# Performance work log

Measured on AMD Instinct MI355X. Metric: run time of the kernel, lower is better.

Reference implementation:

```python
import jax, jax.numpy as jnp
import numpy as np

BATCH, NEURONS, N_FEAT, IN_DIM, OUT_DIM = 256, 1024, 1024, 256, 128


def setup_inputs() -> dict:
    key = jax.random.key(0)
    kx, kg, kv, kw = jax.random.split(key, 4)
    x = jax.random.normal(kx, (BATCH, N_FEAT, IN_DIM), dtype=jnp.float32)
    G = jax.random.normal(kg, (NEURONS, N_FEAT), dtype=jnp.float32)
    # Original initializes v, w to zeros; use randn so outputs/grads are non-trivial.
    v = jax.random.normal(kv, (NEURONS, IN_DIM, OUT_DIM), dtype=jnp.float32)
    w = jax.random.normal(kw, (NEURONS, IN_DIM, OUT_DIM), dtype=jnp.float32)
    return {"x": x, "G": G, "v": v, "w": w}


def reference(x, G, v, w):
    # Original math: out[i,m] = sum_{j,k,l} G[j,k] * x[i,k,l] * (v - w)[j,l,m]
    # Reordered contraction: first G @ x (sum over feature axis k),
    # avoiding the quadratic (batch, neurons, n, in_dim) intermediate.
    Gx = jnp.einsum('jk,ikl->ijl', G, x)          # (batch, neurons, in_dim)
    return jnp.einsum('ijl,jlm->im', Gx, v - w)    # (batch, out_dim)
```

## Files before the change

kernel.cpp:

```cpp
#include <hip/hip_runtime.h>
#include <hip/hip_bf16.h>


typedef __attribute__((ext_vector_type(8))) short bf16x8;
typedef __attribute__((ext_vector_type(4))) float f32x4;

#define AS1C(p) ((const __attribute__((address_space(1))) void*)(p))
#define AS3(p)  ((__attribute__((address_space(3))) void*)(p))

__device__ __forceinline__ unsigned short f2bf(float f) {
    unsigned u = __float_as_uint(f);
    unsigned r = u + 0x7fffu + ((u >> 16) & 1u);
    return (unsigned short)(r >> 16);
}

__global__ void prep_G(const float* __restrict__ G, unsigned short* __restrict__ Gt) {
    __shared__ float tile[32][33];
    int k0 = blockIdx.x * 32, j0 = blockIdx.y * 32;
    int tx = threadIdx.x, ty = threadIdx.y;
    #pragma unroll
    for (int r = 0; r < 32; r += 8)
        tile[ty + r][tx] = G[(size_t)(j0 + ty + r) * 1024 + k0 + tx];
    __syncthreads();
    #pragma unroll
    for (int r = 0; r < 32; r += 8)
        Gt[(size_t)(k0 + ty + r) * 1024 + j0 + tx] = f2bf(tile[tx][ty + r]);
}

__global__ void prep_D(const float* __restrict__ v, const float* __restrict__ w,
                       unsigned short* __restrict__ Dt) {
    __shared__ unsigned short tile[64][132];
    int j0 = blockIdx.x * 64;
    int l  = blockIdx.y;
    int t  = threadIdx.x;
    #pragma unroll
    for (int it = 0; it < 8; ++it) {
        int f = it * 256 + t;
        int j = f >> 5;
        int c4 = (f & 31) * 4;
        size_t g = (size_t)(j0 + j) * 32768 + (size_t)l * 128 + c4;
        float4 a = *(const float4*)(v + g);
        float4 b = *(const float4*)(w + g);
        unsigned short h[4] = { f2bf(a.x - b.x), f2bf(a.y - b.y),
                                f2bf(a.z - b.z), f2bf(a.w - b.w) };
        *(uint2*)(&tile[j][c4]) = *(uint2*)h;
    }
    __syncthreads();
    int m = t >> 1, half = t & 1;
    unsigned short vals[32];
    #pragma unroll
    for (int q = 0; q < 32; ++q) vals[q] = tile[half * 32 + q][m];
    size_t dst = ((size_t)m * 256 + l) * 1024 + j0 + half * 32;
    #pragma unroll
    for (int p = 0; p < 4; ++p)
        *(uint4*)(Dt + dst + p * 8) = *(uint4*)(vals + p * 8);
}

__global__ __launch_bounds__(256) void gemm1(const unsigned short* __restrict__ Gt,
                                             const unsigned short* __restrict__ Dt,
                                             unsigned short* __restrict__ Tt) {
    __shared__ __align__(16) unsigned short As[128 * 32];
    __shared__ __align__(16) unsigned short Bs[128 * 32];
    __shared__ __align__(16) unsigned short Ct[64][136];
    int tid = threadIdx.x, wv = tid >> 6, lane = tid & 63;
    int k0 = blockIdx.x * 128, n0 = blockIdx.y * 128;
    int ldrow = lane >> 2, ldcol = (lane & 3) * 8;
    int wr = (wv >> 1) * 64, wc = (wv & 1) * 64;
    int quad = lane >> 4, l15 = lane & 15;

    f32x4 acc[4][4] = {};

    for (int j0 = 0; j0 < 1024; j0 += 32) {
        #pragma unroll
        for (int i = 0; i < 2; ++i) {
            int r = wv * 32 + i * 16;
            __builtin_amdgcn_global_load_lds(
                AS1C(Gt + (size_t)(k0 + r + ldrow) * 1024 + j0 + ldcol),
                AS3(As + r * 32), 16, 0, 0);
            __builtin_amdgcn_global_load_lds(
                AS1C(Dt + (size_t)(n0 + r + ldrow) * 1024 + j0 + ldcol),
                AS3(Bs + r * 32), 16, 0, 0);
        }
        __syncthreads();
        bf16x8 a[4], b[4];
        #pragma unroll
        for (int rt = 0; rt < 4; ++rt)
            a[rt] = *(const bf16x8*)(As + (wr + rt * 16 + l15) * 32 + quad * 8);
        #pragma unroll
        for (int ct = 0; ct < 4; ++ct)
            b[ct] = *(const bf16x8*)(Bs + (wc + ct * 16 + l15) * 32 + quad * 8);
        #pragma unroll
        for (int rt = 0; rt < 4; ++rt)
            #pragma unroll
            for (int ct = 0; ct < 4; ++ct)
                acc[rt][ct] = __builtin_amdgcn_mfma_f32_16x16x32_bf16(a[rt], b[ct], acc[rt][ct], 0, 0, 0);
        __syncthreads();
    }
    int mQ = n0 >> 8, l0 = n0 & 255;
    #pragma unroll
    for (int h = 0; h < 2; ++h) {
        if ((wv >> 1) == h) {
            #pragma unroll
            for (int rt = 0; rt < 4; ++rt)
                #pragma unroll
                for (int ct = 0; ct < 4; ++ct)
                    #pragma unroll
                    for (int r = 0; r < 4; ++r)
                        Ct[rt * 16 + quad * 4 + r][wc + ct * 16 + l15] = f2bf(acc[rt][ct][r]);
        }
        __syncthreads();
        int row = tid >> 2, qo = (tid & 3) * 32;
        size_t dst = (size_t)mQ * 262144 + (size_t)(k0 + h * 64 + row) * 256 + l0 + qo;
        uint4 d0 = *(uint4*)(&Ct[row][qo]);
        uint4 d1 = *(uint4*)(&Ct[row][qo + 8]);
        uint4 d2 = *(uint4*)(&Ct[row][qo + 16]);
        uint4 d3 = *(uint4*)(&Ct[row][qo + 24]);
        *(uint4*)(Tt + dst)      = d0;
        *(uint4*)(Tt + dst + 8)  = d1;
        *(uint4*)(Tt + dst + 16) = d2;
        *(uint4*)(Tt + dst + 24) = d3;
        __syncthreads();
    }
}

__global__ __launch_bounds__(256, 4) void gemm2(const float* __restrict__ x,
                                                const unsigned short* __restrict__ Tt,
                                                float* __restrict__ out) {
    __shared__ __align__(16) unsigned short Xs[64 * 32];
    __shared__ __align__(16) unsigned short Ts[128 * 32];
    int tid = threadIdx.x, wv = tid >> 6, lane = tid & 63;
    int i0 = blockIdx.x * 64;
    size_t kl0 = (size_t)blockIdx.y * 1024;
    int ldrow = lane >> 2, ldcol = (lane & 3) * 8;
    int wr = (wv >> 1) * 32, wc = (wv & 1) * 64;
    int quad = lane >> 4, l15 = lane & 15;

    f32x4 acc[2][4] = {};

    for (int it = 0; it < 32; ++it) {
        size_t kk = kl0 + it * 32;
        #pragma unroll
        for (int i = 0; i < 2; ++i) {
            int r = wv * 32 + i * 16;
            __builtin_amdgcn_global_load_lds(
                AS1C(Tt + (size_t)(r + ldrow) * 262144 + kk + ldcol),
                AS3(Ts + r * 32), 16, 0, 0);
        }
        #pragma unroll
        for (int i = 0; i < 2; ++i) {
            int f = tid + i * 256;
            int r = f >> 3, c = (f & 7) * 4;
            float4 xv = *(const float4*)(x + (size_t)(i0 + r) * 262144 + kk + c);
            unsigned short h[4] = { f2bf(xv.x), f2bf(xv.y), f2bf(xv.z), f2bf(xv.w) };
            *(uint2*)(Xs + r * 32 + c) = *(uint2*)h;
        }
        __syncthreads();
        bf16x8 a[2], b[4];
        #pragma unroll
        for (int rt = 0; rt < 2; ++rt)
            a[rt] = *(const bf16x8*)(Xs + (wr + rt * 16 + l15) * 32 + quad * 8);
        #pragma unroll
        for (int ct = 0; ct < 4; ++ct)
            b[ct] = *(const bf16x8*)(Ts + (wc + ct * 16 + l15) * 32 + quad * 8);
        #pragma unroll
        for (int rt = 0; rt < 2; ++rt)
            #pragma unroll
            for (int ct = 0; ct < 4; ++ct)
                acc[rt][ct] = __builtin_amdgcn_mfma_f32_16x16x32_bf16(a[rt], b[ct], acc[rt][ct], 0, 0, 0);
        __syncthreads();
    }
    #pragma unroll
    for (int rt = 0; rt < 2; ++rt)
        #pragma unroll
        for (int ct = 0; ct < 4; ++ct)
            #pragma unroll
            for (int r = 0; r < 4; ++r) {
                int i  = i0 + wr + rt * 16 + quad * 4 + r;
                int mo = wc + ct * 16 + l15;
                atomicAdd(&out[(size_t)i * 128 + mo], acc[rt][ct][r]);
            }
}

extern "C" void kernel_launch(void* const* d_in, const int* in_sizes, int n_in,
                              void* d_out, int out_size, void* d_ws, size_t ws_size,
                              hipStream_t stream) {
    const float* x = (const float*)d_in[0];
    const float* G = (const float*)d_in[1];
    const float* v = (const float*)d_in[2];
    const float* w = (const float*)d_in[3];
    float* out = (float*)d_out;

    char* ws = (char*)d_ws;
    unsigned short* Dt = (unsigned short*)(ws);
    unsigned short* Tt = (unsigned short*)(ws + 67108864);
    unsigned short* Gt = (unsigned short*)(ws + 134217728);

    hipMemsetAsync(d_out, 0, (size_t)256 * 128 * sizeof(float), stream);
    prep_G<<<dim3(32, 32), dim3(32, 8), 0, stream>>>(G, Gt);
    prep_D<<<dim3(16, 256), 256, 0, stream>>>(v, w, Dt);
    gemm1<<<dim3(8, 256), 256, 0, stream>>>(Gt, Dt, Tt);
    gemm2<<<dim3(4, 256), 256, 0, stream>>>(x, Tt, out);
}
```

Before: 701.4 us.

## Replace atomic accumulation with partial buffers and reduction; reorder grids; alias LDS

gemm2 stops issuing float atomicAdds to the output. Each block now writes its partial tile to a workspace buffer, and a new reduce_P kernel sums the 256 partials for each output element. This also removes the output memset. The grid axes of gemm1 and gemm2 are swapped so that neighbouring blocks share different operands in cache. gemm1's LDS staging buffers are aliased with the epilogue tile to cut shared memory per block. gemm2's occupancy hint is dropped. The cost is an extra kernel launch plus about 32 MB of partial writes and reads.

```diff
diff --git a/kernel.cpp b/kernel.cpp
--- a/kernel.cpp
+++ b/kernel.cpp
@@ -59,11 +59,13 @@
 __global__ __launch_bounds__(256) void gemm1(const unsigned short* __restrict__ Gt,
                                              const unsigned short* __restrict__ Dt,
                                              unsigned short* __restrict__ Tt) {
-    __shared__ __align__(16) unsigned short As[128 * 32];
-    __shared__ __align__(16) unsigned short Bs[128 * 32];
-    __shared__ __align__(16) unsigned short Ct[64][136];
+    __shared__ __align__(16) char smem[17408];
+    unsigned short* As = (unsigned short*)smem;
+    unsigned short* Bs = As + 4096;
+    unsigned short (*Ct)[136] = (unsigned short (*)[136])smem;
+
     int tid = threadIdx.x, wv = tid >> 6, lane = tid & 63;
-    int k0 = blockIdx.x * 128, n0 = blockIdx.y * 128;
+    int n0 = blockIdx.x * 128, k0 = blockIdx.y * 128;
     int ldrow = lane >> 2, ldcol = (lane & 3) * 8;
     int wr = (wv >> 1) * 64, wc = (wv & 1) * 64;
     int quad = lane >> 4, l15 = lane & 15;
@@ -123,14 +125,14 @@
     }
 }
 
-__global__ __launch_bounds__(256, 4) void gemm2(const float* __restrict__ x,
-                                                const unsigned short* __restrict__ Tt,
-                                                float* __restrict__ out) {
+__global__ __launch_bounds__(256) void gemm2(const float* __restrict__ x,
+                                             const unsigned short* __restrict__ Tt,
+                                             float* __restrict__ P) {
     __shared__ __align__(16) unsigned short Xs[64 * 32];
     __shared__ __align__(16) unsigned short Ts[128 * 32];
     int tid = threadIdx.x, wv = tid >> 6, lane = tid & 63;
-    int i0 = blockIdx.x * 64;
-    size_t kl0 = (size_t)blockIdx.y * 1024;
+    int i0 = blockIdx.y * 64;
+    size_t kl0 = (size_t)blockIdx.x * 1024;
     int ldrow = lane >> 2, ldcol = (lane & 3) * 8;
     int wr = (wv >> 1) * 32, wc = (wv & 1) * 64;
     int quad = lane >> 4, l15 = lane & 15;
@@ -169,16 +171,32 @@
                 acc[rt][ct] = __builtin_amdgcn_mfma_f32_16x16x32_bf16(a[rt], b[ct], acc[rt][ct], 0, 0, 0);
         __syncthreads();
     }
+    float* Pb = P + ((size_t)blockIdx.y * 256 + blockIdx.x) * 8192;
     #pragma unroll
     for (int rt = 0; rt < 2; ++rt)
         #pragma unroll
         for (int ct = 0; ct < 4; ++ct)
             #pragma unroll
             for (int r = 0; r < 4; ++r) {
-                int i  = i0 + wr + rt * 16 + quad * 4 + r;
+                int il = wr + rt * 16 + quad * 4 + r;
                 int mo = wc + ct * 16 + l15;
-                atomicAdd(&out[(size_t)i * 128 + mo], acc[rt][ct][r]);
+                Pb[il * 128 + mo] = acc[rt][ct][r];
             }
+}
+
+__global__ void reduce_P(const float* __restrict__ P, float* __restrict__ out) {
+    int t = blockIdx.x * 256 + threadIdx.x;
+    int i = t >> 7, m = t & 127;
+    const float* p = P + (size_t)(i >> 6) * 256 * 8192 + (size_t)(i & 63) * 128 + m;
+    float s0 = 0.f, s1 = 0.f, s2 = 0.f, s3 = 0.f;
+    #pragma unroll 4
+    for (int c = 0; c < 256; c += 4) {
+        s0 += p[(size_t)(c + 0) * 8192];
+        s1 += p[(size_t)(c + 1) * 8192];
+        s2 += p[(size_t)(c + 2) * 8192];
+        s3 += p[(size_t)(c + 3) * 8192];
+    }
+    out[t] = (s0 + s1) + (s2 + s3);
 }
 
 extern "C" void kernel_launch(void* const* d_in, const int* in_sizes, int n_in,
@@ -194,10 +212,11 @@
     unsigned short* Dt = (unsigned short*)(ws);
     unsigned short* Tt = (unsigned short*)(ws + 67108864);
     unsigned short* Gt = (unsigned short*)(ws + 134217728);
-
-    hipMemsetAsync(d_out, 0, (size_t)256 * 128 * sizeof(float), stream);
+    float*          P  = (float*)(ws + 136314880);
+
     prep_G<<<dim3(32, 32), dim3(32, 8), 0, stream>>>(G, Gt);
     prep_D<<<dim3(16, 256), 256, 0, stream>>>(v, w, Dt);
-    gemm1<<<dim3(8, 256), 256, 0, stream>>>(Gt, Dt, Tt);
-    gemm2<<<dim3(4, 256), 256, 0, stream>>>(x, Tt, out);
-}
+    gemm1<<<dim3(256, 8), 256, 0, stream>>>(Gt, Dt, Tt);
+    gemm2<<<dim3(256, 4), 256, 0, stream>>>(x, Tt, P);
+    reduce_P<<<128, 256, 0, stream>>>(P, out);
+}
```

Measured after the change: 736.6 us. 1.05x slower.
